# Kernel optimization log

Hardware: AMD Instinct MI355X
Metric: run time of the kernel (lower is better)

Reference implementation:

```python
import jax, jax.numpy as jnp
import numpy as np

N, C, K, R = 16384, 64, 16, 4  # points, channels, knn neighbors, upsample ratio


def setup_inputs() -> dict:
    key = jax.random.key(0)
    k1, k2 = jax.random.split(key, 2)
    x = jax.random.normal(k1, (N, C), dtype=jnp.float32)
    # EdgeConv MLP: Linear(2*C -> C*R)
    W = jax.random.normal(k2, (2 * C, C * R), dtype=jnp.float32) / np.sqrt(2 * C)
    b = jnp.zeros((C * R,), dtype=jnp.float32)
    return {"x": x, "W": W, "b": b}


def knn_idx(x, k):
    # pairwise squared distances, self excluded (knn_graph default loop=False)
    sq = jnp.sum(x * x, axis=1)                      # [N]
    d = sq[:, None] + sq[None, :] - 2.0 * (x @ x.T)  # [N, N]
    n = x.shape[0]
    d = d.at[jnp.arange(n), jnp.arange(n)].set(jnp.inf)
    _, idx = jax.lax.top_k(-d, k)                    # [N, k] nearest neighbors
    return idx


def reference(x, W, b):
    idx = knn_idx(x, K)                 # [N, K] int32 neighbor indices
    x_j = x[idx]                        # [N, K, C] gathered neighbor features
    x_i = x[:, None, :]                 # [N, 1, C]
    # EdgeConv message: MLP([x_i, x_j - x_i]) with ReLU, then max-aggregate
    feat = jnp.concatenate([jnp.broadcast_to(x_i, x_j.shape), x_j - x_i], axis=-1)  # [N, K, 2C]
    h = jax.nn.relu(feat @ W + b)       # [N, K, C*R]
    out = jnp.max(h, axis=1)            # [N, C*R]
    # PointSuffle: out[n, c*R + s] -> y[n*R + s, c]
    y = out.reshape(N, C, R).transpose(0, 2, 1).reshape(N * R, C)
    return y
```

## Files before the change

kernel.cpp:

```cpp
#include <hip/hip_runtime.h>

#define NPTS 16384
#define CDIM 64

using bf16x8 = __attribute__((ext_vector_type(8))) short;
using s16x4  = __attribute__((ext_vector_type(4))) short;
using f32x4  = __attribute__((ext_vector_type(4))) float;
using i32x4  = __attribute__((ext_vector_type(4))) int;

static __device__ __forceinline__ float b2f(short h){
  unsigned u = ((unsigned)(unsigned short)h) << 16;
  return __builtin_bit_cast(float, u);
}
static __device__ __forceinline__ short f2b(float f){
  unsigned u = __builtin_bit_cast(unsigned, f);
  u = (u + 0x7fffu + ((u >> 16) & 1u)) >> 16;
  return (short)u;
}
static __device__ __forceinline__ int dpp_shr1_i(int x){
  return __builtin_amdgcn_update_dpp(x, x, 0x111, 0xF, 0xF, false);
}
static __device__ __forceinline__ float dpp_shr1_f(float x){
  int r = dpp_shr1_i(__builtin_bit_cast(int, x));
  return __builtin_bit_cast(float, r);
}

__global__ __launch_bounds__(256) void k_prep(const float* __restrict__ xf,
    short* __restrict__ xh, float* __restrict__ sq05){
  const int tid = threadIdx.x;
  const int row = blockIdx.x*64 + (tid >> 2);
  const int part = tid & 3;
  const float* p = xf + row*CDIM + part*16;
  float ps = 0.f;
  bf16x8 vh0, vh1;
  #pragma unroll
  for (int e = 0; e < 8; ++e){
    float f = p[e];
    vh0[e] = f2b(f);
    ps = fmaf(f, f, ps);
  }
  #pragma unroll
  for (int e = 0; e < 8; ++e){
    float f = p[8 + e];
    vh1[e] = f2b(f);
    ps = fmaf(f, f, ps);
  }
  *(bf16x8*)(xh + row*CDIM + part*16)     = vh0;
  *(bf16x8*)(xh + row*CDIM + part*16 + 8) = vh1;
  ps += __shfl_down(ps, 2);
  ps += __shfl_down(ps, 1);
  if (part == 0) sq05[row] = 0.5f * ps;
}

__global__ __launch_bounds__(256) void k_wprep(const float* __restrict__ Wf,
    short* __restrict__ WtG){
  const int n = threadIdx.x;
  const int kq = blockIdx.x;
  const int chunk = (kq >> 1) ^ (n & 15);
  s16x4 v;
  #pragma unroll
  for (int e = 0; e < 4; ++e) v[e] = f2b(Wf[(kq*4 + e)*256 + n]);
  *(s16x4*)(WtG + n*128 + chunk*8 + (kq & 1)*4) = v;
}

__global__ __launch_bounds__(256) void k_knn(const short* __restrict__ xh,
    const float* __restrict__ sq05, int* __restrict__ cand){
  __shared__ __align__(16) short Bh[2][128*72];
  __shared__ float sqt[2][128];
  const int tid = threadIdx.x, lane = tid & 63, w = tid >> 6;
  const int l15 = lane & 15, quad = lane >> 4;
  const int q = blockIdx.x & 3, ib = blockIdx.x >> 2;
  const int rb = ib*64 + w*16;
  const int jbase = q*4096;
  const int thrsrc = (lane & 48) | 15;
  const bool notl0 = (l15 != 0);

  bf16x8 ah[2];
  #pragma unroll
  for (int ks = 0; ks < 2; ++ks)
    ah[ks] = *(const bf16x8*)(xh + (rb + l15)*CDIM + ks*32 + quad*8);

  float lv[4]; int li[4]; float thr[4];
  #pragma unroll
  for (int r = 0; r < 4; ++r){
    lv[r] = __builtin_inff(); li[r] = 0; thr[r] = __builtin_inff();
  }

  #pragma unroll
  for (int g = 0; g < 4; ++g){
    int c = g*256 + tid, row = c >> 3, seg = c & 7;
    *(bf16x8*)(&Bh[0][row*72 + seg*8]) =
        *(const bf16x8*)(xh + (jbase + row)*CDIM + seg*8);
  }
  if (tid < 128) sqt[0][tid] = sq05[jbase + tid];
  __syncthreads();

  #pragma unroll 1
  for (int t = 0; t < 32; ++t){
    const int cur = t & 1;
    const int j0 = jbase + t*128;
    if (t < 31){
      const int jn = j0 + 128;
      #pragma unroll
      for (int g = 0; g < 4; ++g){
        int c = g*256 + tid, row = c >> 3, seg = c & 7;
        *(bf16x8*)(&Bh[cur^1][row*72 + seg*8]) =
            *(const bf16x8*)(xh + (jn + row)*CDIM + seg*8);
      }
      if (tid < 128) sqt[cur^1][tid] = sq05[jn + tid];
    }

    f32x4 acc[8];
    #pragma unroll
    for (int js = 0; js < 8; ++js) acc[js] = (f32x4){0.f,0.f,0.f,0.f};
    #pragma unroll
    for (int ks = 0; ks < 2; ++ks){
      #pragma unroll
      for (int js = 0; js < 8; ++js){
        bf16x8 bh = *(const bf16x8*)(&Bh[cur][(js*16 + l15)*72 + (ks*4 + quad)*8]);
        acc[js] = __builtin_amdgcn_mfma_f32_16x16x32_bf16(ah[ks], bh, acc[js], 0,0,0);
      }
    }

    #pragma unroll
    for (int js = 0; js < 8; ++js){
      float sqv = sqt[cur][js*16 + l15];
      float s4[4];
      unsigned long long bal[4];
      #pragma unroll
      for (int r = 0; r < 4; ++r){
        s4[r] = sqv - acc[js][r];
        bal[r] = __ballot(s4[r] < thr[r]);
      }
      #pragma unroll
      for (int r = 0; r < 4; ++r){
        if (bal[r]){
          unsigned qb = (unsigned)((bal[r] >> (quad*16)) & 0xffffull);
          while (qb){
            int jj = __builtin_ctz(qb); qb &= qb - 1u;
            float cv = __shfl(s4[r], quad*16 + jj);
            int   cj = j0 + js*16 + jj;
            float lp = dpp_shr1_f(lv[r]);
            int   ip = dpp_shr1_i(li[r]);
            bool c1 = (cv < lv[r]);
            bool c0 = notl0 && (cv < lp);
            float iv = c0 ? lp : cv;
            int   ii = c0 ? ip : cj;
            if (c1){ lv[r] = iv; li[r] = ii; }
          }
          thr[r] = __shfl(lv[r], thrsrc);
        }
      }
    }
    __syncthreads();
  }

  #pragma unroll
  for (int r = 0; r < 4; ++r)
    cand[(rb + quad*4 + r)*64 + q*16 + l15] = li[r];
}

__global__ __launch_bounds__(256) void k_sel(const float* __restrict__ xf,
    const float* __restrict__ sq05, const int* __restrict__ cand,
    int* __restrict__ nbr){
  const int lane = threadIdx.x & 63, w = threadIdx.x >> 6;
  const int i = blockIdx.x*4 + w;
  int idx = cand[i*64 + lane] & (NPTS - 1);

  const f32x4* pi4 = (const f32x4*)(xf + i*CDIM);
  const f32x4* pj4 = (const f32x4*)(xf + idx*CDIM);
  f32x4 a4 = (f32x4){0.f,0.f,0.f,0.f};
  #pragma unroll
  for (int e = 0; e < 16; ++e){
    f32x4 va = pi4[e], vb = pj4[e];
    #pragma unroll
    for (int c = 0; c < 4; ++c) a4[c] = fmaf(va[c], vb[c], a4[c]);
  }
  float dot = (a4[0] + a4[1]) + (a4[2] + a4[3]);
  float v = fmaf(-2.f, dot, 2.f*(sq05[i] + sq05[idx]));
  if (idx == i) v = __builtin_inff();

  #pragma unroll
  for (int k = 2; k <= 64; k <<= 1){
    #pragma unroll
    for (int j = k >> 1; j > 0; j >>= 1){
      float pv = __shfl_xor(v, j); int pi = __shfl_xor(idx, j);
      bool dir = ((lane & k) == 0);
      bool lower = ((lane & j) == 0);
      bool pless = (pv < v) || (pv == v && pi < idx);
      bool take = (lower == dir) ? pless : !pless;
      if (take){ v = pv; idx = pi; }
    }
  }
  if (lane < 16) nbr[i*16 + lane] = idx;
}

__global__ __launch_bounds__(256) void k_mlp(const float* __restrict__ xf,
    const short* __restrict__ WtG, const float* __restrict__ bfp,
    const int* __restrict__ nbr, float* __restrict__ y){
  __shared__ __align__(16) short Wt[256*128];
  const int tid = threadIdx.x, lane = tid & 63, w = tid >> 6;
  const int l15 = lane & 15, quad = lane >> 4;
  for (int c = tid; c < 4096; c += 256)
    ((i32x4*)Wt)[c] = ((const i32x4*)WtG)[c];
  __syncthreads();
  const int ibase = blockIdx.x*32 + w*8;

  #pragma unroll 1
  for (int it = 0; it < 4; ++it){
    const int ia = ibase + it*2, ib2 = ia + 1;
    const int nba = nbr[ia*16  + l15] & (NPTS - 1);
    const int nbb = nbr[ib2*16 + l15] & (NPTS - 1);
    bf16x8 afa[4], afb[4];
    {
      const float* xi = xf + ia*CDIM;
      const float* xj = xf + nba*CDIM;
      f32x4 a0 = *(const f32x4*)(xi + quad*8),      a1 = *(const f32x4*)(xi + quad*8 + 4);
      f32x4 a2 = *(const f32x4*)(xi + 32 + quad*8), a3 = *(const f32x4*)(xi + 32 + quad*8 + 4);
      f32x4 b0 = *(const f32x4*)(xj + quad*8),      b1 = *(const f32x4*)(xj + quad*8 + 4);
      f32x4 b2 = *(const f32x4*)(xj + 32 + quad*8), b3 = *(const f32x4*)(xj + 32 + quad*8 + 4);
      #pragma unroll
      for (int e = 0; e < 4; ++e){
        afa[0][e] = f2b(a0[e]); afa[0][4+e] = f2b(a1[e]);
        afa[1][e] = f2b(a2[e]); afa[1][4+e] = f2b(a3[e]);
        afa[2][e] = f2b(b0[e] - a0[e]); afa[2][4+e] = f2b(b1[e] - a1[e]);
        afa[3][e] = f2b(b2[e] - a2[e]); afa[3][4+e] = f2b(b3[e] - a3[e]);
      }
    }
    {
      const float* xi = xf + ib2*CDIM;
      const float* xj = xf + nbb*CDIM;
      f32x4 a0 = *(const f32x4*)(xi + quad*8),      a1 = *(const f32x4*)(xi + quad*8 + 4);
      f32x4 a2 = *(const f32x4*)(xi + 32 + quad*8), a3 = *(const f32x4*)(xi + 32 + quad*8 + 4);
      f32x4 b0 = *(const f32x4*)(xj + quad*8),      b1 = *(const f32x4*)(xj + quad*8 + 4);
      f32x4 b2 = *(const f32x4*)(xj + 32 + quad*8), b3 = *(const f32x4*)(xj + 32 + quad*8 + 4);
      #pragma unroll
      for (int e = 0; e < 4; ++e){
        afb[0][e] = f2b(a0[e]); afb[0][4+e] = f2b(a1[e]);
        afb[1][e] = f2b(a2[e]); afb[1][4+e] = f2b(a3[e]);
        afb[2][e] = f2b(b0[e] - a0[e]); afb[2][4+e] = f2b(b1[e] - a1[e]);
        afb[3][e] = f2b(b2[e] - a2[e]); afb[3][4+e] = f2b(b3[e] - a3[e]);
      }
    }

    #pragma unroll
    for (int half = 0; half < 2; ++half){
      f32x4 aca[8], acb[8];
      #pragma unroll
      for (int n = 0; n < 8; ++n){
        aca[n] = (f32x4){0.f,0.f,0.f,0.f};
        acb[n] = (f32x4){0.f,0.f,0.f,0.f};
      }
      #pragma unroll
      for (int ks = 0; ks < 4; ++ks){
        #pragma unroll
        for (int ntl = 0; ntl < 8; ++ntl){
          int nt = half*8 + ntl;
          int chunkS = ((ks*4 + quad) ^ l15);
          bf16x8 bfr = *(const bf16x8*)(Wt + (nt*16 + l15)*128 + chunkS*8);
          aca[ntl] = __builtin_amdgcn_mfma_f32_16x16x32_bf16(afa[ks], bfr, aca[ntl], 0,0,0);
          acb[ntl] = __builtin_amdgcn_mfma_f32_16x16x32_bf16(afb[ks], bfr, acb[ntl], 0,0,0);
        }
      }
      #pragma unroll
      for (int ntl = 0; ntl < 8; ++ntl){
        int col = (half*8 + ntl)*16 + l15;
        float bv = bfp[col];
        float ma = fmaxf(fmaxf(aca[ntl][0], aca[ntl][1]), fmaxf(aca[ntl][2], aca[ntl][3]));
        ma = fmaxf(ma, __shfl_xor(ma, 16));
        ma = fmaxf(ma, __shfl_xor(ma, 32));
        float mb = fmaxf(fmaxf(acb[ntl][0], acb[ntl][1]), fmaxf(acb[ntl][2], acb[ntl][3]));
        mb = fmaxf(mb, __shfl_xor(mb, 16));
        mb = fmaxf(mb, __shfl_xor(mb, 32));
        if (lane < 16){
          y[(ia*4  + (col & 3))*CDIM + (col >> 2)] = fmaxf(ma + bv, 0.f);
          y[(ib2*4 + (col & 3))*CDIM + (col >> 2)] = fmaxf(mb + bv, 0.f);
        }
      }
    }
  }
}

extern "C" void kernel_launch(void* const* d_in, const int* in_sizes, int n_in,
                              void* d_out, int out_size, void* d_ws, size_t ws_size,
                              hipStream_t stream){
  const float* x    = (const float*)d_in[0];
  const float* Wm   = (const float*)d_in[1];
  const float* bias = (const float*)d_in[2];
  float* y = (float*)d_out;
  char* ws = (char*)d_ws;
  short* xh   = (short*)ws;
  float* sq05 = (float*)(ws + (2 << 20));
  short* WtG  = (short*)(ws + (2 << 20) + (64 << 10));
  int*   cand = (int*)  (ws + (2 << 20) + (128 << 10));
  int*   nbr  = (int*)  (ws + (6 << 20) + (128 << 10));
  (void)in_sizes; (void)n_in; (void)out_size; (void)ws_size;

  k_prep <<<256,  256, 0, stream>>>(x, xh, sq05);
  k_wprep<<<32,   256, 0, stream>>>(Wm, WtG);
  k_knn  <<<1024, 256, 0, stream>>>(xh, sq05, cand);
  k_sel  <<<4096, 256, 0, stream>>>(x, sq05, cand, nbr);
  k_mlp  <<<512,  256, 0, stream>>>(x, WtG, bias, nbr, y);
}
```

Measured before the change: 377.5 us.

## Fuse weight prep into prep kernel and candidate selection into MLP kernel

Merges the W bf16 transpose kernel into the x prep kernel by block-index dispatch, and moves the per-point exact-distance rerank and bitonic sort of the 64 candidates into the MLP kernel. This cuts the pipeline from five launches to three and removes the nbr intermediate buffer round-trip. The selection work now runs inside the MLP blocks, which have only 512 blocks and high LDS use, so the rerank gets less parallelism and may lengthen the MLP critical path.

```diff
diff --git a/kernel.cpp b/kernel.cpp
--- a/kernel.cpp
+++ b/kernel.cpp
@@ -26,41 +26,42 @@
 }
 
 __global__ __launch_bounds__(256) void k_prep(const float* __restrict__ xf,
-    short* __restrict__ xh, float* __restrict__ sq05){
+    const float* __restrict__ Wf, short* __restrict__ xh,
+    float* __restrict__ sq05, short* __restrict__ WtG){
   const int tid = threadIdx.x;
-  const int row = blockIdx.x*64 + (tid >> 2);
-  const int part = tid & 3;
-  const float* p = xf + row*CDIM + part*16;
-  float ps = 0.f;
-  bf16x8 vh0, vh1;
-  #pragma unroll
-  for (int e = 0; e < 8; ++e){
-    float f = p[e];
-    vh0[e] = f2b(f);
-    ps = fmaf(f, f, ps);
-  }
-  #pragma unroll
-  for (int e = 0; e < 8; ++e){
-    float f = p[8 + e];
-    vh1[e] = f2b(f);
-    ps = fmaf(f, f, ps);
-  }
-  *(bf16x8*)(xh + row*CDIM + part*16)     = vh0;
-  *(bf16x8*)(xh + row*CDIM + part*16 + 8) = vh1;
-  ps += __shfl_down(ps, 2);
-  ps += __shfl_down(ps, 1);
-  if (part == 0) sq05[row] = 0.5f * ps;
-}
-
-__global__ __launch_bounds__(256) void k_wprep(const float* __restrict__ Wf,
-    short* __restrict__ WtG){
-  const int n = threadIdx.x;
-  const int kq = blockIdx.x;
-  const int chunk = (kq >> 1) ^ (n & 15);
-  s16x4 v;
-  #pragma unroll
-  for (int e = 0; e < 4; ++e) v[e] = f2b(Wf[(kq*4 + e)*256 + n]);
-  *(s16x4*)(WtG + n*128 + chunk*8 + (kq & 1)*4) = v;
+  const int b = blockIdx.x;
+  if (b < 256){
+    const int row = b*64 + (tid >> 2);
+    const int part = tid & 3;
+    const float* p = xf + row*CDIM + part*16;
+    float ps = 0.f;
+    bf16x8 vh0, vh1;
+    #pragma unroll
+    for (int e = 0; e < 8; ++e){
+      float f = p[e];
+      vh0[e] = f2b(f);
+      ps = fmaf(f, f, ps);
+    }
+    #pragma unroll
+    for (int e = 0; e < 8; ++e){
+      float f = p[8 + e];
+      vh1[e] = f2b(f);
+      ps = fmaf(f, f, ps);
+    }
+    *(bf16x8*)(xh + row*CDIM + part*16)     = vh0;
+    *(bf16x8*)(xh + row*CDIM + part*16 + 8) = vh1;
+    ps += __shfl_down(ps, 2);
+    ps += __shfl_down(ps, 1);
+    if (part == 0) sq05[row] = 0.5f * ps;
+  } else {
+    const int kq = b - 256;
+    const int n = tid;
+    const int chunk = (kq >> 1) ^ (n & 15);
+    s16x4 v;
+    #pragma unroll
+    for (int e = 0; e < 4; ++e) v[e] = f2b(Wf[(kq*4 + e)*256 + n]);
+    *(s16x4*)(WtG + n*128 + chunk*8 + (kq & 1)*4) = v;
+  }
 }
 
 __global__ __launch_bounds__(256) void k_knn(const short* __restrict__ xh,
@@ -160,44 +161,10 @@
     cand[(rb + quad*4 + r)*64 + q*16 + l15] = li[r];
 }
 
-__global__ __launch_bounds__(256) void k_sel(const float* __restrict__ xf,
-    const float* __restrict__ sq05, const int* __restrict__ cand,
-    int* __restrict__ nbr){
-  const int lane = threadIdx.x & 63, w = threadIdx.x >> 6;
-  const int i = blockIdx.x*4 + w;
-  int idx = cand[i*64 + lane] & (NPTS - 1);
-
-  const f32x4* pi4 = (const f32x4*)(xf + i*CDIM);
-  const f32x4* pj4 = (const f32x4*)(xf + idx*CDIM);
-  f32x4 a4 = (f32x4){0.f,0.f,0.f,0.f};
-  #pragma unroll
-  for (int e = 0; e < 16; ++e){
-    f32x4 va = pi4[e], vb = pj4[e];
-    #pragma unroll
-    for (int c = 0; c < 4; ++c) a4[c] = fmaf(va[c], vb[c], a4[c]);
-  }
-  float dot = (a4[0] + a4[1]) + (a4[2] + a4[3]);
-  float v = fmaf(-2.f, dot, 2.f*(sq05[i] + sq05[idx]));
-  if (idx == i) v = __builtin_inff();
-
-  #pragma unroll
-  for (int k = 2; k <= 64; k <<= 1){
-    #pragma unroll
-    for (int j = k >> 1; j > 0; j >>= 1){
-      float pv = __shfl_xor(v, j); int pi = __shfl_xor(idx, j);
-      bool dir = ((lane & k) == 0);
-      bool lower = ((lane & j) == 0);
-      bool pless = (pv < v) || (pv == v && pi < idx);
-      bool take = (lower == dir) ? pless : !pless;
-      if (take){ v = pv; idx = pi; }
-    }
-  }
-  if (lane < 16) nbr[i*16 + lane] = idx;
-}
-
 __global__ __launch_bounds__(256) void k_mlp(const float* __restrict__ xf,
-    const short* __restrict__ WtG, const float* __restrict__ bfp,
-    const int* __restrict__ nbr, float* __restrict__ y){
+    const float* __restrict__ sq05, const short* __restrict__ WtG,
+    const float* __restrict__ bfp, const int* __restrict__ cand,
+    float* __restrict__ y){
   __shared__ __align__(16) short Wt[256*128];
   const int tid = threadIdx.x, lane = tid & 63, w = tid >> 6;
   const int l15 = lane & 15, quad = lane >> 4;
@@ -209,8 +176,39 @@
   #pragma unroll 1
   for (int it = 0; it < 4; ++it){
     const int ia = ibase + it*2, ib2 = ia + 1;
-    const int nba = nbr[ia*16  + l15] & (NPTS - 1);
-    const int nbb = nbr[ib2*16 + l15] & (NPTS - 1);
+    int nba, nbb;
+    #pragma unroll
+    for (int pt = 0; pt < 2; ++pt){
+      const int i = pt ? ib2 : ia;
+      int idx = cand[i*64 + lane] & (NPTS - 1);
+      const f32x4* pi4 = (const f32x4*)(xf + i*CDIM);
+      const f32x4* pj4 = (const f32x4*)(xf + idx*CDIM);
+      f32x4 a4 = (f32x4){0.f,0.f,0.f,0.f};
+      #pragma unroll
+      for (int e = 0; e < 16; ++e){
+        f32x4 va = pi4[e], vb = pj4[e];
+        #pragma unroll
+        for (int c = 0; c < 4; ++c) a4[c] = fmaf(va[c], vb[c], a4[c]);
+      }
+      float dot = (a4[0] + a4[1]) + (a4[2] + a4[3]);
+      float v = fmaf(-2.f, dot, 2.f*(sq05[i] + sq05[idx]));
+      if (idx == i) v = __builtin_inff();
+      #pragma unroll
+      for (int k = 2; k <= 64; k <<= 1){
+        #pragma unroll
+        for (int j = k >> 1; j > 0; j >>= 1){
+          float pv = __shfl_xor(v, j); int pi = __shfl_xor(idx, j);
+          bool dir = ((lane & k) == 0);
+          bool lower = ((lane & j) == 0);
+          bool pless = (pv < v) || (pv == v && pi < idx);
+          bool take = (lower == dir) ? pless : !pless;
+          if (take){ v = pv; idx = pi; }
+        }
+      }
+      int nb = __shfl(idx, l15) & (NPTS - 1);
+      if (pt) nbb = nb; else nba = nb;
+    }
+
     bf16x8 afa[4], afb[4];
     {
       const float* xi = xf + ia*CDIM;
@@ -293,12 +291,9 @@
   float* sq05 = (float*)(ws + (2 << 20));
   short* WtG  = (short*)(ws + (2 << 20) + (64 << 10));
   int*   cand = (int*)  (ws + (2 << 20) + (128 << 10));
-  int*   nbr  = (int*)  (ws + (6 << 20) + (128 << 10));
   (void)in_sizes; (void)n_in; (void)out_size; (void)ws_size;
 
-  k_prep <<<256,  256, 0, stream>>>(x, xh, sq05);
-  k_wprep<<<32,   256, 0, stream>>>(Wm, WtG);
-  k_knn  <<<1024, 256, 0, stream>>>(xh, sq05, cand);
-  k_sel  <<<4096, 256, 0, stream>>>(x, sq05, cand, nbr);
-  k_mlp  <<<512,  256, 0, stream>>>(x, WtG, bias, nbr, y);
-}
+  k_prep<<<288,  256, 0, stream>>>(x, Wm, xh, sq05, WtG);
+  k_knn <<<1024, 256, 0, stream>>>(xh, sq05, cand);
+  k_mlp <<<512,  256, 0, stream>>>(x, sq05, WtG, bias, cand, y);
+}
```

New measurement: 387.9 us. +2.8%, slower.
